# Kernel optimization log

Measured on AMD Instinct MI355X. Metric: run time of the kernel, lower is better.

## Reference

```python
import jax, jax.numpy as jnp
import numpy as np

B, C, H, W, K = 8, 256, 128, 128, 19  # batch, image channels, spatial, num keypoints


def _uniform_linear(key, out_dim, in_dim):
    # torch nn.Linear default init: U(-1/sqrt(fan_in), 1/sqrt(fan_in))
    bound = 1.0 / np.sqrt(in_dim)
    kw, kb = jax.random.split(key)
    w = jax.random.uniform(kw, (out_dim, in_dim), jnp.float32, -bound, bound)
    b = jax.random.uniform(kb, (out_dim,), jnp.float32, -bound, bound)
    return w, b


def setup_inputs() -> dict:
    key = jax.random.key(0)
    ks = jax.random.split(key, 8)
    image_features = jax.random.normal(ks[0], (B, C, H, W), jnp.float32)
    # keypoints: (x, y, vis). forward computes int((x / W).clamp(0, W-1)), so
    # coords are drawn in [0, W*W) / [0, H*H) to cover the full heatmap grid.
    kx = jax.random.uniform(ks[1], (B, K), jnp.float32, 0.0, float(W * W))
    ky = jax.random.uniform(ks[2], (B, K), jnp.float32, 0.0, float(H * H))
    vis = jax.random.uniform(ks[3], (B, K), jnp.float32)  # >0 => visible
    keypoint_features = jnp.stack([kx, ky, vis], axis=-1)  # [B,K,3]
    img_fc_w, img_fc_b = _uniform_linear(ks[4], C, C)
    kp_proj_w, kp_proj_b = _uniform_linear(ks[5], K, K)  # 1x1 conv == K->K linear over channels
    kp_fc_w, kp_fc_b = _uniform_linear(ks[6], C, K)
    attn_fc_w, attn_fc_b = _uniform_linear(ks[7], 1, C)
    return {
        "image_features": image_features,
        "keypoint_features": keypoint_features,
        "img_fc_w": img_fc_w, "img_fc_b": img_fc_b,
        "kp_proj_w": kp_proj_w, "kp_proj_b": kp_proj_b,
        "kp_fc_w": kp_fc_w, "kp_fc_b": kp_fc_b,
        "attn_fc_w": attn_fc_w, "attn_fc_b": attn_fc_b,
    }


def keypoints_to_heatmap(keypoints, Hh, Ww):
    # Vectorized version of the original nested Python double-loop scatter.
    bsz, nkp, _ = keypoints.shape
    vis = (keypoints[:, :, 2] > 0).astype(jnp.float32)            # [B,K]
    # clamp to [0, dim-1] then truncate to int (values are >=0 so floor==trunc)
    x = jnp.clip(keypoints[:, :, 0] / Ww, 0.0, Ww - 1).astype(jnp.int32)  # [B,K]
    y = jnp.clip(keypoints[:, :, 1] / Hh, 0.0, Hh - 1).astype(jnp.int32)  # [B,K]
    bi = jnp.arange(bsz)[:, None]
    ki = jnp.arange(nkp)[None, :]
    heatmap = jnp.zeros((bsz, nkp, Hh, Ww), jnp.float32)
    # one write per (b,k) -> indices unique across writes; add of 0 for invisible kp
    return heatmap.at[bi, ki, y, x].add(vis)


def reference(image_features, keypoint_features,
              img_fc_w, img_fc_b, kp_proj_w, kp_proj_b,
              kp_fc_w, kp_fc_b, attn_fc_w, attn_fc_b):
    bsz, nch, Hh, Ww = image_features.shape
    heatmap = keypoints_to_heatmap(keypoint_features, Hh, Ww)  # [B,K,H,W]
    # F.interpolate to the same (H,W) with bilinear/align_corners=False maps
    # output pixel i -> input coord i exactly => identity; no-op.
    # keypoint_proj: 1x1 conv over K channels == per-pixel K->K linear
    kp_feat = jnp.einsum('bkhw,ok->bohw', heatmap, kp_proj_w) + kp_proj_b[None, :, None, None]
    img = image_features.reshape(bsz, nch, Hh * Ww).transpose(0, 2, 1)   # [B,S,C]
    kp = kp_feat.reshape(bsz, K, Hh * Ww).transpose(0, 2, 1)             # [B,S,K]
    img_proj = jnp.einsum('bsc,oc->bso', img, img_fc_w) + img_fc_b       # [B,S,C]
    kp_proj = jnp.einsum('bsk,ok->bso', kp, kp_fc_w) + kp_fc_b           # [B,S,C]
    combined = jnp.tanh(img_proj + kp_proj)
    scores = jax.nn.sigmoid(jnp.einsum('bsc,oc->bso', combined, attn_fc_w) + attn_fc_b)  # [B,S,1]
    attended = img * scores                                              # [B,S,C]
    return attended.transpose(0, 2, 1).reshape(bsz, nch, Hh, Ww)
```

## Files before the change

### kernel.cpp

```cpp
#include <hip/hip_runtime.h>
#include <hip/hip_bf16.h>

#define CCH 256
#define HH 128
#define WW 128
#define SS (HH*WW)
#define NB 8
#define NK 19
#define STILE 64

typedef __attribute__((ext_vector_type(8))) short short8v;
typedef __attribute__((ext_vector_type(4))) float f32x4;

static __device__ __forceinline__ unsigned short f2bf(float x) {
    __hip_bfloat16 h = __float2bfloat16(x);
    return *reinterpret_cast<unsigned short*>(&h);
}
static __device__ __forceinline__ float bf2f(unsigned short u) {
    union { unsigned int i; float f; } z; z.i = ((unsigned int)u) << 16; return z.f;
}
static __device__ __forceinline__ float tanh_fast(float x) {
    float e = __expf(2.f * x);
    return 1.f - 2.f / (e + 1.f);
}

__global__ __launch_bounds__(256) void precompute_kernel(
    const float* __restrict__ kf,
    const float* __restrict__ img_fc_w,
    const float* __restrict__ img_fc_b,
    const float* __restrict__ kp_proj_w,
    const float* __restrict__ kp_proj_b,
    const float* __restrict__ kp_fc_w,
    const float* __restrict__ kp_fc_b,
    float* __restrict__ cb,
    float* __restrict__ delta,
    int* __restrict__ pix,
    unsigned short* __restrict__ Wfrag)
{
    int t = threadIdx.x;
    {
        float acc = img_fc_b[t] + kp_fc_b[t];
        for (int k2 = 0; k2 < NK; ++k2) acc += kp_fc_w[t * NK + k2] * kp_proj_b[k2];
        cb[t] = acc;
        for (int k = 0; k < NK; ++k) {
            float d = 0.f;
            for (int k2 = 0; k2 < NK; ++k2) d += kp_fc_w[t * NK + k2] * kp_proj_w[k2 * NK + k];
            delta[t * NK + k] = d;
        }
    }
    if (t < NB * NK) {
        float kx = kf[t * 3 + 0], ky = kf[t * 3 + 1], vis = kf[t * 3 + 2];
        int p = -1;
        if (vis > 0.f) {
            int xi = (int)fminf(fmaxf(kx * (1.f / (float)WW), 0.f), (float)(WW - 1));
            int yi = (int)fminf(fmaxf(ky * (1.f / (float)HH), 0.f), (float)(HH - 1));
            p = yi * WW + xi;
        }
        pix[t] = p;
    }
    for (int g = t; g < 8 * 16 * 64; g += 256) {
        int lane = g & 63;
        int ot = (g >> 6) & 15;
        int ks = g >> 10;
        int o = ot * 16 + (lane & 15);
        int c0 = ks * 32 + (lane >> 4) * 8;
#pragma unroll
        for (int j = 0; j < 8; ++j)
            Wfrag[g * 8 + j] = f2bf(img_fc_w[o * CCH + c0 + j]);
    }
}

__global__ __launch_bounds__(512, 4) void main_kernel(
    const float* __restrict__ img,
    const unsigned short* __restrict__ Wfrag,
    const float* __restrict__ cb,
    const float* __restrict__ aw,
    const float* __restrict__ attn_b,
    float* __restrict__ out)
{
    __shared__ unsigned short Xl[64 * 256];
    __shared__ float partial[8][64];
    __shared__ float scl[64];

    const int t = threadIdx.x;
    const int l = t & 63;
    const int w = t >> 6;
    const int bid = blockIdx.x;
    const int b = bid >> 8;
    const int sb = (bid & 255) * STILE;
    const float* imgb = img + (size_t)b * CCH * SS;

    const int sl = t & 63;
    const int c0 = (t >> 6) * 32;

    {
        float xf[32];
#pragma unroll
        for (int j = 0; j < 32; ++j)
            xf[j] = imgb[(size_t)(c0 + j) * SS + sb + sl];
#pragma unroll
        for (int jb = 0; jb < 4; ++jb) {
            short8v pk;
#pragma unroll
            for (int e = 0; e < 8; ++e) pk[e] = (short)f2bf(xf[jb * 8 + e]);
            int cblk = (c0 >> 3) + jb;
            int idx = sl * 256 + ((cblk ^ (sl & 7)) << 3);
            *reinterpret_cast<short8v*>(&Xl[idx]) = pk;
        }
    }
    __syncthreads();

    f32x4 acc[2][4];
#pragma unroll
    for (int m = 0; m < 2; ++m)
#pragma unroll
        for (int n = 0; n < 4; ++n)
            acc[m][n] = (f32x4){0.f, 0.f, 0.f, 0.f};

#pragma unroll
    for (int ks = 0; ks < 8; ++ks) {
        short8v a[2], bf[4];
#pragma unroll
        for (int m = 0; m < 2; ++m) {
            int ot = w * 2 + m;
            a[m] = *reinterpret_cast<const short8v*>(
                &Wfrag[(((ks * 16 + ot) * 64) + l) * 8]);
        }
#pragma unroll
        for (int n = 0; n < 4; ++n) {
            int s = n * 16 + (l & 15);
            int cblk = ks * 4 + (l >> 4);
            int idx = s * 256 + ((cblk ^ (s & 7)) << 3);
            bf[n] = *reinterpret_cast<const short8v*>(&Xl[idx]);
        }
#pragma unroll
        for (int m = 0; m < 2; ++m)
#pragma unroll
            for (int n = 0; n < 4; ++n)
                acc[m][n] = __builtin_amdgcn_mfma_f32_16x16x32_bf16(a[m], bf[n], acc[m][n], 0, 0, 0);
    }

    float p4[4];
#pragma unroll
    for (int n = 0; n < 4; ++n) {
        float accp = 0.f;
#pragma unroll
        for (int m = 0; m < 2; ++m)
#pragma unroll
            for (int r = 0; r < 4; ++r) {
                int o = (w * 2 + m) * 16 + ((l >> 4) << 2) + r;
                accp += aw[o] * tanh_fast(acc[m][n][r] + cb[o]);
            }
        accp += __shfl_xor(accp, 16);
        accp += __shfl_xor(accp, 32);
        p4[n] = accp;
    }
    if (l < 16) {
#pragma unroll
        for (int n = 0; n < 4; ++n) partial[w][n * 16 + l] = p4[n];
    }
    __syncthreads();
    if (t < 64) {
        float z = attn_b[0];
#pragma unroll
        for (int ww = 0; ww < 8; ++ww) z += partial[ww][t];
        scl[t] = 1.f / (1.f + __expf(-z));
    }
    __syncthreads();

    {
        float sc = scl[sl];
#pragma unroll
        for (int jb = 0; jb < 4; ++jb) {
            int cblk = (c0 >> 3) + jb;
            int idx = sl * 256 + ((cblk ^ (sl & 7)) << 3);
            short8v v = *reinterpret_cast<const short8v*>(&Xl[idx]);
#pragma unroll
            for (int e = 0; e < 8; ++e)
                out[(size_t)(b * CCH + c0 + jb * 8 + e) * SS + sb + sl] =
                    bf2f((unsigned short)v[e]) * sc;
        }
    }
}

__global__ __launch_bounds__(256) void fixup_kernel(
    const float* __restrict__ img,
    const float* __restrict__ img_fc_w,
    const float* __restrict__ aw,
    const float* __restrict__ attn_b,
    const float* __restrict__ cb,
    const float* __restrict__ delta,
    const int* __restrict__ pix,
    float* __restrict__ out)
{
    int bk = blockIdx.x;
    int b = bk / NK;
    int p = pix[bk];
    if (p < 0) return;
    __shared__ float x[256];
    __shared__ float red[256];
    __shared__ float ssc;
    int t = threadIdx.x;
    const float* imgb = img + (size_t)b * CCH * SS;
    x[t] = imgb[(size_t)t * SS + p];
    __syncthreads();
    float dsum = 0.f;
    for (int k2 = 0; k2 < NK; ++k2)
        if (pix[b * NK + k2] == p) dsum += delta[t * NK + k2];
    float acc = cb[t] + dsum;
    for (int c = 0; c < CCH; ++c) acc += img_fc_w[t * CCH + c] * x[c];
    red[t] = aw[t] * tanh_fast(acc);
    __syncthreads();
    for (int off = 128; off > 0; off >>= 1) {
        if (t < off) red[t] += red[t + off];
        __syncthreads();
    }
    if (t == 0) ssc = 1.f / (1.f + __expf(-(red[0] + attn_b[0])));
    __syncthreads();
    out[(size_t)(b * CCH + t) * SS + p] = x[t] * ssc;
}

extern "C" void kernel_launch(void* const* d_in, const int* in_sizes, int n_in,
                              void* d_out, int out_size, void* d_ws, size_t ws_size,
                              hipStream_t stream) {
    (void)in_sizes; (void)n_in; (void)out_size; (void)ws_size;
    const float* img       = (const float*)d_in[0];
    const float* kf        = (const float*)d_in[1];
    const float* img_fc_w  = (const float*)d_in[2];
    const float* img_fc_b  = (const float*)d_in[3];
    const float* kp_proj_w = (const float*)d_in[4];
    const float* kp_proj_b = (const float*)d_in[5];
    const float* kp_fc_w   = (const float*)d_in[6];
    const float* kp_fc_b   = (const float*)d_in[7];
    const float* attn_fc_w = (const float*)d_in[8];
    const float* attn_fc_b = (const float*)d_in[9];
    float* out = (float*)d_out;

    char* ws = (char*)d_ws;
    float* cb             = (float*)(ws);
    float* delta          = (float*)(ws + 1024);
    int*   pix            = (int*)  (ws + 20480);
    unsigned short* Wfrag = (unsigned short*)(ws + 21504);

    precompute_kernel<<<1, 256, 0, stream>>>(kf, img_fc_w, img_fc_b, kp_proj_w,
                                             kp_proj_b, kp_fc_w, kp_fc_b,
                                             cb, delta, pix, Wfrag);
    main_kernel<<<NB * (SS / STILE), 512, 0, stream>>>(img, Wfrag, cb,
                                                       attn_fc_w, attn_fc_b, out);
    fixup_kernel<<<NB * NK, 256, 0, stream>>>(img, img_fc_w, attn_fc_w, attn_fc_b,
                                              cb, delta, pix, out);
}
```

Before: 92.98 us.

## Make main kernel persistent over multiple tiles with double-buffered LDS prefetch

Each block now processes 8 spatial tiles of 32 positions instead of one 64-position tile. It keeps the bf16 weight fragments resident in registers across tiles, and stages cb and the attention weights in LDS. The next tile's global loads are issued before the current tile's MFMA work, into a second LDS buffer, to overlap memory latency with compute and to amortize weight loads. The cost is fewer blocks (512 vs 2048), higher register pressure from holding 16 weight fragments per thread, and a stray dummy LDS self-assignment.

```diff
diff --git a/kernel.cpp b/kernel.cpp
--- a/kernel.cpp
+++ b/kernel.cpp
@@ -7,7 +7,10 @@
 #define SS (HH*WW)
 #define NB 8
 #define NK 19
-#define STILE 64
+#define STILE 32
+#define TPB 8
+#define NTILES (NB * (SS / STILE))
+#define NBLK (NTILES / TPB)
 
 typedef __attribute__((ext_vector_type(8))) short short8v;
 typedef __attribute__((ext_vector_type(4))) float f32x4;
@@ -78,108 +81,139 @@
     const float* __restrict__ attn_b,
     float* __restrict__ out)
 {
-    __shared__ unsigned short Xl[64 * 256];
-    __shared__ float partial[8][64];
-    __shared__ float scl[64];
+    __shared__ unsigned short Xl[2][STILE * 256];
+    __shared__ float partial[8][STILE];
+    __shared__ float cbl[256];
+    __shared__ float awl[256];
 
     const int t = threadIdx.x;
     const int l = t & 63;
     const int w = t >> 6;
-    const int bid = blockIdx.x;
-    const int b = bid >> 8;
-    const int sb = (bid & 255) * STILE;
-    const float* imgb = img + (size_t)b * CCH * SS;
-
-    const int sl = t & 63;
-    const int c0 = (t >> 6) * 32;
-
+    const int sl = t & 31;
+    const int cg = t >> 5;
+    const int c0 = cg * 16;
+
+    short8v a[2][8];
+#pragma unroll
+    for (int ks = 0; ks < 8; ++ks)
+#pragma unroll
+        for (int m = 0; m < 2; ++m)
+            a[m][ks] = *reinterpret_cast<const short8v*>(
+                &Wfrag[(((ks * 16 + (w * 2 + m)) * 64) + l) * 8]);
+
+    if (t < 256) { cbl[t] = cb[t]; awl[t] = aw[t]; }
+    const float attnb = attn_b[0];
+
+    const int tile0 = blockIdx.x * TPB;
+
+    float xf[16];
     {
-        float xf[32];
-#pragma unroll
-        for (int j = 0; j < 32; ++j)
-            xf[j] = imgb[(size_t)(c0 + j) * SS + sb + sl];
-#pragma unroll
-        for (int jb = 0; jb < 4; ++jb) {
+        int tile = tile0;
+        const float* imgb = img + (size_t)(tile >> 9) * CCH * SS + (tile & 511) * STILE;
+#pragma unroll
+        for (int j = 0; j < 16; ++j)
+            xf[j] = imgb[(size_t)(c0 + j) * SS + sl];
+#pragma unroll
+        for (int jb = 0; jb < 2; ++jb) {
             short8v pk;
 #pragma unroll
             for (int e = 0; e < 8; ++e) pk[e] = (short)f2bf(xf[jb * 8 + e]);
-            int cblk = (c0 >> 3) + jb;
-            int idx = sl * 256 + ((cblk ^ (sl & 7)) << 3);
-            *reinterpret_cast<short8v*>(&Xl[idx]) = pk;
-        }
-    }
-    __syncthreads();
-
-    f32x4 acc[2][4];
-#pragma unroll
-    for (int m = 0; m < 2; ++m)
-#pragma unroll
-        for (int n = 0; n < 4; ++n)
-            acc[m][n] = (f32x4){0.f, 0.f, 0.f, 0.f};
-
-#pragma unroll
-    for (int ks = 0; ks < 8; ++ks) {
-        short8v a[2], bf[4];
-#pragma unroll
-        for (int m = 0; m < 2; ++m) {
-            int ot = w * 2 + m;
-            a[m] = *reinterpret_cast<const short8v*>(
-                &Wfrag[(((ks * 16 + ot) * 64) + l) * 8]);
-        }
-#pragma unroll
-        for (int n = 0; n < 4; ++n) {
-            int s = n * 16 + (l & 15);
-            int cblk = ks * 4 + (l >> 4);
-            int idx = s * 256 + ((cblk ^ (s & 7)) << 3);
-            bf[n] = *reinterpret_cast<const short8v*>(&Xl[idx]);
-        }
+            int cblk = cg * 2 + jb;
+            Xl[0][0] = Xl[0][0];
+            *reinterpret_cast<short8v*>(
+                &Xl[0][sl * 256 + ((cblk ^ (sl & 7)) << 3)]) = pk;
+        }
+    }
+
+    int cur = 0;
+    for (int it = 0; it < TPB; ++it) {
+        const int tile = tile0 + it;
+        const int b = tile >> 9;
+        const int sb = (tile & 511) * STILE;
+
+        if (it + 1 < TPB) {
+            const int tn = tile + 1;
+            const float* imgn = img + (size_t)(tn >> 9) * CCH * SS + (tn & 511) * STILE;
+#pragma unroll
+            for (int j = 0; j < 16; ++j)
+                xf[j] = imgn[(size_t)(c0 + j) * SS + sl];
+        }
+
+        __syncthreads();
+
+        const unsigned short* Xc = &Xl[cur][0];
+        f32x4 acc[2][2];
 #pragma unroll
         for (int m = 0; m < 2; ++m)
 #pragma unroll
-            for (int n = 0; n < 4; ++n)
-                acc[m][n] = __builtin_amdgcn_mfma_f32_16x16x32_bf16(a[m], bf[n], acc[m][n], 0, 0, 0);
-    }
-
-    float p4[4];
-#pragma unroll
-    for (int n = 0; n < 4; ++n) {
-        float accp = 0.f;
-#pragma unroll
-        for (int m = 0; m < 2; ++m)
-#pragma unroll
-            for (int r = 0; r < 4; ++r) {
-                int o = (w * 2 + m) * 16 + ((l >> 4) << 2) + r;
-                accp += aw[o] * tanh_fast(acc[m][n][r] + cb[o]);
-            }
-        accp += __shfl_xor(accp, 16);
-        accp += __shfl_xor(accp, 32);
-        p4[n] = accp;
-    }
-    if (l < 16) {
-#pragma unroll
-        for (int n = 0; n < 4; ++n) partial[w][n * 16 + l] = p4[n];
-    }
-    __syncthreads();
-    if (t < 64) {
-        float z = attn_b[0];
-#pragma unroll
-        for (int ww = 0; ww < 8; ++ww) z += partial[ww][t];
-        scl[t] = 1.f / (1.f + __expf(-z));
-    }
-    __syncthreads();
-
-    {
-        float sc = scl[sl];
-#pragma unroll
-        for (int jb = 0; jb < 4; ++jb) {
-            int cblk = (c0 >> 3) + jb;
-            int idx = sl * 256 + ((cblk ^ (sl & 7)) << 3);
-            short8v v = *reinterpret_cast<const short8v*>(&Xl[idx]);
+            for (int n = 0; n < 2; ++n)
+                acc[m][n] = (f32x4){0.f, 0.f, 0.f, 0.f};
+
+#pragma unroll
+        for (int ks = 0; ks < 8; ++ks) {
+            const int cblk = ks * 4 + (l >> 4);
+            const int s0 = (l & 15);
+            const int s1 = 16 + s0;
+            short8v bf0 = *reinterpret_cast<const short8v*>(
+                &Xc[s0 * 256 + ((cblk ^ (s0 & 7)) << 3)]);
+            short8v bf1 = *reinterpret_cast<const short8v*>(
+                &Xc[s1 * 256 + ((cblk ^ (s1 & 7)) << 3)]);
+            acc[0][0] = __builtin_amdgcn_mfma_f32_16x16x32_bf16(a[0][ks], bf0, acc[0][0], 0, 0, 0);
+            acc[1][0] = __builtin_amdgcn_mfma_f32_16x16x32_bf16(a[1][ks], bf0, acc[1][0], 0, 0, 0);
+            acc[0][1] = __builtin_amdgcn_mfma_f32_16x16x32_bf16(a[0][ks], bf1, acc[0][1], 0, 0, 0);
+            acc[1][1] = __builtin_amdgcn_mfma_f32_16x16x32_bf16(a[1][ks], bf1, acc[1][1], 0, 0, 0);
+        }
+
+        float p2[2];
+#pragma unroll
+        for (int n = 0; n < 2; ++n) {
+            float accp = 0.f;
+#pragma unroll
+            for (int m = 0; m < 2; ++m)
+#pragma unroll
+                for (int r = 0; r < 4; ++r) {
+                    int o = (w * 2 + m) * 16 + ((l >> 4) << 2) + r;
+                    accp += awl[o] * tanh_fast(acc[m][n][r] + cbl[o]);
+                }
+            accp += __shfl_xor(accp, 16);
+            accp += __shfl_xor(accp, 32);
+            p2[n] = accp;
+        }
+        if (l < 16) {
+            partial[w][l] = p2[0];
+            partial[w][16 + l] = p2[1];
+        }
+        __syncthreads();
+
+        float z = attnb;
+#pragma unroll
+        for (int ww = 0; ww < 8; ++ww) z += partial[ww][sl];
+        float sc = 1.f / (1.f + __expf(-z));
+
+#pragma unroll
+        for (int jb = 0; jb < 2; ++jb) {
+            int cblk = cg * 2 + jb;
+            short8v v = *reinterpret_cast<const short8v*>(
+                &Xc[sl * 256 + ((cblk ^ (sl & 7)) << 3)]);
 #pragma unroll
             for (int e = 0; e < 8; ++e)
                 out[(size_t)(b * CCH + c0 + jb * 8 + e) * SS + sb + sl] =
                     bf2f((unsigned short)v[e]) * sc;
         }
+
+        if (it + 1 < TPB) {
+            unsigned short* Xn = &Xl[cur ^ 1][0];
+#pragma unroll
+            for (int jb = 0; jb < 2; ++jb) {
+                short8v pk;
+#pragma unroll
+                for (int e = 0; e < 8; ++e) pk[e] = (short)f2bf(xf[jb * 8 + e]);
+                int cblk = cg * 2 + jb;
+                *reinterpret_cast<short8v*>(
+                    &Xn[sl * 256 + ((cblk ^ (sl & 7)) << 3)]) = pk;
+            }
+        }
+        cur ^= 1;
     }
 }
 
@@ -245,8 +279,8 @@
     precompute_kernel<<<1, 256, 0, stream>>>(kf, img_fc_w, img_fc_b, kp_proj_w,
                                              kp_proj_b, kp_fc_w, kp_fc_b,
                                              cb, delta, pix, Wfrag);
-    main_kernel<<<NB * (SS / STILE), 512, 0, stream>>>(img, Wfrag, cb,
-                                                       attn_fc_w, attn_fc_b, out);
+    main_kernel<<<NBLK, 512, 0, stream>>>(img, Wfrag, cb,
+                                          attn_fc_w, attn_fc_b, out);
     fixup_kernel<<<NB * NK, 256, 0, stream>>>(img, img_fc_w, attn_fc_w, attn_fc_b,
                                               cb, delta, pix, out);
 }
```

After: 188.7 us. 2.03x slower.

## Restructure main kernel to single-wave 16-pixel tiles with register-resident activations

Applied to the files above, without the earlier changes.

Replaces the 512-thread, 64-pixel blocks that staged the image tile in LDS with 64-thread single-wave blocks covering 16 pixels. Each lane loads its activation fragments straight into registers as MFMA B operands, and runs all 16 output tiles over the full K. This removes the LDS staging, the cross-wave partial reduction and two barriers. The scale is reduced with shuffles only. It also interleaves block-to-tile mapping, packs bias and attention weight into a float2 LDS table, and uses hardware reciprocal in tanh and sigmoid. In exchange, each wave now re-reads the whole weight fragment set from global/L2 for only 16 pixels, and the per-lane accumulator and register use grow.

```diff
diff --git a/kernel.cpp b/kernel.cpp
--- a/kernel.cpp
+++ b/kernel.cpp
@@ -7,7 +7,8 @@
 #define SS (HH*WW)
 #define NB 8
 #define NK 19
-#define STILE 64
+#define PTILE 16
+#define NTIL (NB * (SS / PTILE))
 
 typedef __attribute__((ext_vector_type(8))) short short8v;
 typedef __attribute__((ext_vector_type(4))) float f32x4;
@@ -21,7 +22,10 @@
 }
 static __device__ __forceinline__ float tanh_fast(float x) {
     float e = __expf(2.f * x);
-    return 1.f - 2.f / (e + 1.f);
+    return 1.f - 2.f * __builtin_amdgcn_rcpf(e + 1.f);
+}
+static __device__ __forceinline__ float sigmoid_fast(float z) {
+    return __builtin_amdgcn_rcpf(1.f + __expf(-z));
 }
 
 __global__ __launch_bounds__(256) void precompute_kernel(
@@ -32,16 +36,19 @@
     const float* __restrict__ kp_proj_b,
     const float* __restrict__ kp_fc_w,
     const float* __restrict__ kp_fc_b,
+    const float* __restrict__ attn_fc_w,
     float* __restrict__ cb,
     float* __restrict__ delta,
     int* __restrict__ pix,
-    unsigned short* __restrict__ Wfrag)
+    unsigned short* __restrict__ Wfrag,
+    float2* __restrict__ cw2)
 {
     int t = threadIdx.x;
     {
         float acc = img_fc_b[t] + kp_fc_b[t];
         for (int k2 = 0; k2 < NK; ++k2) acc += kp_fc_w[t * NK + k2] * kp_proj_b[k2];
         cb[t] = acc;
+        cw2[t] = make_float2(acc, attn_fc_w[t]);
         for (int k = 0; k < NK; ++k) {
             float d = 0.f;
             for (int k2 = 0; k2 < NK; ++k2) d += kp_fc_w[t * NK + k2] * kp_proj_w[k2 * NK + k];
@@ -60,9 +67,9 @@
     }
     for (int g = t; g < 8 * 16 * 64; g += 256) {
         int lane = g & 63;
-        int ot = (g >> 6) & 15;
+        int m = (g >> 6) & 15;
         int ks = g >> 10;
-        int o = ot * 16 + (lane & 15);
+        int o = m * 16 + (lane & 15);
         int c0 = ks * 32 + (lane >> 4) * 8;
 #pragma unroll
         for (int j = 0; j < 8; ++j)
@@ -70,117 +77,85 @@
     }
 }
 
-__global__ __launch_bounds__(512, 4) void main_kernel(
+__global__ __launch_bounds__(64, 4) void main_kernel(
     const float* __restrict__ img,
     const unsigned short* __restrict__ Wfrag,
-    const float* __restrict__ cb,
-    const float* __restrict__ aw,
+    const float2* __restrict__ cw2,
     const float* __restrict__ attn_b,
     float* __restrict__ out)
 {
-    __shared__ unsigned short Xl[64 * 256];
-    __shared__ float partial[8][64];
-    __shared__ float scl[64];
-
-    const int t = threadIdx.x;
-    const int l = t & 63;
-    const int w = t >> 6;
+    __shared__ float2 cwl[256];
+
+    const int l = threadIdx.x;
     const int bid = blockIdx.x;
-    const int b = bid >> 8;
-    const int sb = (bid & 255) * STILE;
+    const int swz = (bid & 7) * (NTIL / 8) + (bid >> 3);
+    const int b = swz >> 10;
+    const int px0 = (swz & 1023) * PTILE;
     const float* imgb = img + (size_t)b * CCH * SS;
-
-    const int sl = t & 63;
-    const int c0 = (t >> 6) * 32;
+    float* outb = out + (size_t)b * CCH * SS;
+
+    const int sg = px0 + (l & 15);
+    const int cg8 = (l >> 4) * 8;
 
     {
-        float xf[32];
-#pragma unroll
-        for (int j = 0; j < 32; ++j)
-            xf[j] = imgb[(size_t)(c0 + j) * SS + sb + sl];
-#pragma unroll
-        for (int jb = 0; jb < 4; ++jb) {
-            short8v pk;
-#pragma unroll
-            for (int e = 0; e < 8; ++e) pk[e] = (short)f2bf(xf[jb * 8 + e]);
-            int cblk = (c0 >> 3) + jb;
-            int idx = sl * 256 + ((cblk ^ (sl & 7)) << 3);
-            *reinterpret_cast<short8v*>(&Xl[idx]) = pk;
+        const float4* src = reinterpret_cast<const float4*>(cw2);
+        float4* dst = reinterpret_cast<float4*>(cwl);
+        dst[l] = src[l];
+        dst[l + 64] = src[l + 64];
+    }
+    __syncthreads();
+
+    float xf[8][8];
+#pragma unroll
+    for (int ks = 0; ks < 8; ++ks)
+#pragma unroll
+        for (int j = 0; j < 8; ++j)
+            xf[ks][j] = imgb[(size_t)(ks * 32 + cg8 + j) * SS + sg];
+
+    short8v bfr[8];
+#pragma unroll
+    for (int ks = 0; ks < 8; ++ks) {
+        short8v pk;
+#pragma unroll
+        for (int j = 0; j < 8; ++j) pk[j] = (short)f2bf(xf[ks][j]);
+        bfr[ks] = pk;
+    }
+
+    f32x4 acc[16];
+#pragma unroll
+    for (int m = 0; m < 16; ++m) acc[m] = (f32x4){0.f, 0.f, 0.f, 0.f};
+
+#pragma unroll
+    for (int ks = 0; ks < 8; ++ks) {
+#pragma unroll
+        for (int m = 0; m < 16; ++m) {
+            short8v a = *reinterpret_cast<const short8v*>(
+                &Wfrag[(((ks * 16 + m) * 64) + l) * 8]);
+            acc[m] = __builtin_amdgcn_mfma_f32_16x16x32_bf16(a, bfr[ks], acc[m], 0, 0, 0);
         }
     }
-    __syncthreads();
-
-    f32x4 acc[2][4];
-#pragma unroll
-    for (int m = 0; m < 2; ++m)
-#pragma unroll
-        for (int n = 0; n < 4; ++n)
-            acc[m][n] = (f32x4){0.f, 0.f, 0.f, 0.f};
-
-#pragma unroll
-    for (int ks = 0; ks < 8; ++ks) {
-        short8v a[2], bf[4];
-#pragma unroll
-        for (int m = 0; m < 2; ++m) {
-            int ot = w * 2 + m;
-            a[m] = *reinterpret_cast<const short8v*>(
-                &Wfrag[(((ks * 16 + ot) * 64) + l) * 8]);
-        }
-#pragma unroll
-        for (int n = 0; n < 4; ++n) {
-            int s = n * 16 + (l & 15);
-            int cblk = ks * 4 + (l >> 4);
-            int idx = s * 256 + ((cblk ^ (s & 7)) << 3);
-            bf[n] = *reinterpret_cast<const short8v*>(&Xl[idx]);
-        }
-#pragma unroll
-        for (int m = 0; m < 2; ++m)
-#pragma unroll
-            for (int n = 0; n < 4; ++n)
-                acc[m][n] = __builtin_amdgcn_mfma_f32_16x16x32_bf16(a[m], bf[n], acc[m][n], 0, 0, 0);
-    }
-
-    float p4[4];
-#pragma unroll
-    for (int n = 0; n < 4; ++n) {
-        float accp = 0.f;
-#pragma unroll
-        for (int m = 0; m < 2; ++m)
-#pragma unroll
-            for (int r = 0; r < 4; ++r) {
-                int o = (w * 2 + m) * 16 + ((l >> 4) << 2) + r;
-                accp += aw[o] * tanh_fast(acc[m][n][r] + cb[o]);
-            }
-        accp += __shfl_xor(accp, 16);
-        accp += __shfl_xor(accp, 32);
-        p4[n] = accp;
-    }
-    if (l < 16) {
-#pragma unroll
-        for (int n = 0; n < 4; ++n) partial[w][n * 16 + l] = p4[n];
-    }
-    __syncthreads();
-    if (t < 64) {
-        float z = attn_b[0];
-#pragma unroll
-        for (int ww = 0; ww < 8; ++ww) z += partial[ww][t];
-        scl[t] = 1.f / (1.f + __expf(-z));
-    }
-    __syncthreads();
-
-    {
-        float sc = scl[sl];
-#pragma unroll
-        for (int jb = 0; jb < 4; ++jb) {
-            int cblk = (c0 >> 3) + jb;
-            int idx = sl * 256 + ((cblk ^ (sl & 7)) << 3);
-            short8v v = *reinterpret_cast<const short8v*>(&Xl[idx]);
-#pragma unroll
-            for (int e = 0; e < 8; ++e)
-                out[(size_t)(b * CCH + c0 + jb * 8 + e) * SS + sb + sl] =
-                    bf2f((unsigned short)v[e]) * sc;
-        }
-    }
+
+    float z = 0.f;
+#pragma unroll
+    for (int m = 0; m < 16; ++m) {
+        int o4 = m * 16 + ((l >> 4) << 2);
+        float4 q0 = *reinterpret_cast<const float4*>(&cwl[o4]);
+        float4 q1 = *reinterpret_cast<const float4*>(&cwl[o4 + 2]);
+        z += q0.y * tanh_fast(acc[m][0] + q0.x);
+        z += q0.w * tanh_fast(acc[m][1] + q0.z);
+        z += q1.y * tanh_fast(acc[m][2] + q1.x);
+        z += q1.w * tanh_fast(acc[m][3] + q1.z);
+    }
+    z += __shfl_xor(z, 16);
+    z += __shfl_xor(z, 32);
+    float sc = sigmoid_fast(z + attn_b[0]);
+
+#pragma unroll
+    for (int ks = 0; ks < 8; ++ks)
+#pragma unroll
+        for (int j = 0; j < 8; ++j)
+            outb[(size_t)(ks * 32 + cg8 + j) * SS + sg] =
+                bf2f((unsigned short)bfr[ks][j]) * sc;
 }
 
 __global__ __launch_bounds__(256) void fixup_kernel(
@@ -215,7 +190,7 @@
         if (t < off) red[t] += red[t + off];
         __syncthreads();
     }
-    if (t == 0) ssc = 1.f / (1.f + __expf(-(red[0] + attn_b[0])));
+    if (t == 0) ssc = sigmoid_fast(red[0] + attn_b[0]);
     __syncthreads();
     out[(size_t)(b * CCH + t) * SS + p] = x[t] * ssc;
 }
@@ -241,12 +216,12 @@
     float* delta          = (float*)(ws + 1024);
     int*   pix            = (int*)  (ws + 20480);
     unsigned short* Wfrag = (unsigned short*)(ws + 21504);
+    float2* cw2           = (float2*)(ws + 152576);
 
     precompute_kernel<<<1, 256, 0, stream>>>(kf, img_fc_w, img_fc_b, kp_proj_w,
-                                             kp_proj_b, kp_fc_w, kp_fc_b,
-                                             cb, delta, pix, Wfrag);
-    main_kernel<<<NB * (SS / STILE), 512, 0, stream>>>(img, Wfrag, cb,
-                                                       attn_fc_w, attn_fc_b, out);
+                                             kp_proj_b, kp_fc_w, kp_fc_b, attn_fc_w,
+                                             cb, delta, pix, Wfrag, cw2);
+    main_kernel<<<NTIL, 64, 0, stream>>>(img, Wfrag, cw2, attn_fc_b, out);
     fixup_kernel<<<NB * NK, 256, 0, stream>>>(img, img_fc_w, attn_fc_w, attn_fc_b,
                                               cb, delta, pix, out);
 }
```

Measured after the change: 243.4 us. 162% more time.
